# Kernel optimization log

Measured on AMD Instinct MI355X. Metric: run time of the kernel, lower is better.

Reference implementation:

```python
import jax, jax.numpy as jnp
import numpy as np

# Module config (matches FootprintExtruder defaults)
L1_HEIGHT = 0
ROOF_HEIGHT = 1
L1_ID_OFFSET = 0
ROOF_ID_OFFSET = 1
FP_ID_MIN = 100
FP_ID_MAX = 5000
MAX_HEIGHT = 384


def setup_inputs() -> dict:
    key = jax.random.key(0)
    k1, k2 = jax.random.split(key)
    B, H, W = 1, 768, 768
    # assert in forward: max(height_field) < max_height
    height_field = jax.random.randint(k1, (B, H, W), 0, MAX_HEIGHT, dtype=jnp.int32)
    seg_map = jax.random.randint(k2, (B, H, W), 0, FP_ID_MAX, dtype=jnp.int32)
    return {"height_field": height_field, "seg_map": seg_map}


def reference(height_field, seg_map):
    """Extrude 2D height/seg maps into a [B, max_height, H, W] voxel id volume.

    For each column (b, h, w) with height hf and id seg:
      z <  hf and seg in footprint_id_range:
          z <  l1_height            -> seg + l1_id_offset
          z >= hf - roof_height     -> seg + roof_id_offset  (roof voxels)
          otherwise                 -> seg
      z <  hf, seg not a footprint  -> seg
      z >= hf                       -> 0 (empty)
    """
    z = jnp.arange(MAX_HEIGHT, dtype=jnp.int32)[None, :, None, None]  # [1, D, 1, 1]
    hf = height_field[:, None, :, :]   # [B, 1, H, W]
    seg = seg_map[:, None, :, :]       # [B, 1, H, W]

    is_fp = (seg >= FP_ID_MIN) & (seg < FP_ID_MAX)
    fp_id = jnp.where(
        z < L1_HEIGHT, seg + L1_ID_OFFSET,
        jnp.where(z >= hf - ROOF_HEIGHT, seg + ROOF_ID_OFFSET, seg),
    )
    volume = jnp.where(z < hf, jnp.where(is_fp, fp_id, seg), 0)
    return volume.astype(jnp.int32)
```

## Files before the change

kernel.cpp:

```cpp
#include <hip/hip_runtime.h>

#define L1_HEIGHT 0
#define ROOF_HEIGHT 1
#define ROOF_ID_OFFSET 1
#define FP_ID_MIN 100
#define FP_ID_MAX 5000
#define MAX_HEIGHT 384
#define HH 768
#define WW 768
#define HW (HH * WW)

typedef int vint4 __attribute__((ext_vector_type(4)));

__device__ __forceinline__ int voxel(int z, int hf, int seg) {
    bool is_fp = (seg >= FP_ID_MIN) & (seg < FP_ID_MAX);
    int fp = (z >= hf - ROOF_HEIGHT) ? seg + ROOF_ID_OFFSET : seg;
    int v  = is_fp ? fp : seg;
    return (z < hf) ? v : 0;
}

__global__ __launch_bounds__(256) void extrude_kernel(
        const int* __restrict__ hf_map, const int* __restrict__ seg_map,
        int* __restrict__ out) {
    const int p = (blockIdx.x * 256 + threadIdx.x) * 4;
    const int z = blockIdx.y;

    const vint4 hf4 = *(const vint4*)(hf_map  + p);
    const vint4 sg4 = *(const vint4*)(seg_map + p);

    vint4 o;
    o.x = voxel(z, hf4.x, sg4.x);
    o.y = voxel(z, hf4.y, sg4.y);
    o.z = voxel(z, hf4.z, sg4.z);
    o.w = voxel(z, hf4.w, sg4.w);

    __builtin_nontemporal_store(o, (vint4*)(out + (size_t)z * HW + p));
}

extern "C" void kernel_launch(void* const* d_in, const int* in_sizes, int n_in,
                              void* d_out, int out_size, void* d_ws, size_t ws_size,
                              hipStream_t stream) {
    const int* hf  = (const int*)d_in[0];
    const int* seg = (const int*)d_in[1];
    int* out = (int*)d_out;

    dim3 grid(HW / 1024, MAX_HEIGHT);
    extrude_kernel<<<grid, 256, 0, stream>>>(hf, seg, out);
}
```

Baseline: 841.4 us.

## Use grid-stride persistent loop with plain stores and simplified voxel logic

Replaces the 2D grid (one block row per z slice) with a fixed 8192-block grid where each thread loops over flattened (z, pixel) indices, computing z by division. The nontemporal store is replaced with a regular vector store, and the roof test is simplified to an equality check. This is meant to reduce block scheduling overhead and instruction count. The trade-offs are per-iteration integer division, and the loss of the streaming-store hint may increase cache pollution on the large output write.

```diff
diff --git a/kernel.cpp b/kernel.cpp
--- a/kernel.cpp
+++ b/kernel.cpp
@@ -9,32 +9,45 @@
 #define HH 768
 #define WW 768
 #define HW (HH * WW)
+#define HW4 (HW / 4)
+#define N4 (MAX_HEIGHT * HW4)
+
+#define NBLOCKS 8192
+#define NTHREADS (NBLOCKS * 256)
+#define ITERS (N4 / NTHREADS)
 
 typedef int vint4 __attribute__((ext_vector_type(4)));
 
 __device__ __forceinline__ int voxel(int z, int hf, int seg) {
     bool is_fp = (seg >= FP_ID_MIN) & (seg < FP_ID_MAX);
-    int fp = (z >= hf - ROOF_HEIGHT) ? seg + ROOF_ID_OFFSET : seg;
-    int v  = is_fp ? fp : seg;
+    int v = ((z == hf - 1) & is_fp) ? seg + ROOF_ID_OFFSET : seg;
     return (z < hf) ? v : 0;
 }
 
 __global__ __launch_bounds__(256) void extrude_kernel(
         const int* __restrict__ hf_map, const int* __restrict__ seg_map,
         int* __restrict__ out) {
-    const int p = (blockIdx.x * 256 + threadIdx.x) * 4;
-    const int z = blockIdx.y;
+    const unsigned g = blockIdx.x * 256 + threadIdx.x;
 
-    const vint4 hf4 = *(const vint4*)(hf_map  + p);
-    const vint4 sg4 = *(const vint4*)(seg_map + p);
+    #pragma unroll 3
+    for (int k = 0; k < ITERS; ++k) {
+        const unsigned idx = g + (unsigned)k * NTHREADS;
+        const unsigned z   = idx / HW4;
+        const unsigned p4  = idx - z * HW4;
+        const int*     pp  = (const int*)(hf_map  + (size_t)p4 * 4);
+        const int*     sp  = (const int*)(seg_map + (size_t)p4 * 4);
 
-    vint4 o;
-    o.x = voxel(z, hf4.x, sg4.x);
-    o.y = voxel(z, hf4.y, sg4.y);
-    o.z = voxel(z, hf4.z, sg4.z);
-    o.w = voxel(z, hf4.w, sg4.w);
+        const vint4 hf4 = *(const vint4*)pp;
+        const vint4 sg4 = *(const vint4*)sp;
 
-    __builtin_nontemporal_store(o, (vint4*)(out + (size_t)z * HW + p));
+        vint4 o;
+        o.x = voxel((int)z, hf4.x, sg4.x);
+        o.y = voxel((int)z, hf4.y, sg4.y);
+        o.z = voxel((int)z, hf4.z, sg4.z);
+        o.w = voxel((int)z, hf4.w, sg4.w);
+
+        *(vint4*)(out + (size_t)idx * 4) = o;
+    }
 }
 
 extern "C" void kernel_launch(void* const* d_in, const int* in_sizes, int n_in,
@@ -44,6 +57,5 @@
     const int* seg = (const int*)d_in[1];
     int* out = (int*)d_out;
 
-    dim3 grid(HW / 1024, MAX_HEIGHT);
-    extrude_kernel<<<grid, 256, 0, stream>>>(hf, seg, out);
+    extrude_kernel<<<dim3(NBLOCKS), 256, 0, stream>>>(hf, seg, out);
 }
```

Result: slower. 890.0 us (+5.8%).
